# Kernel tuning notes

Measured on AMD Instinct MI355X. Metric: run time of the kernel, lower is better.

## Reference

```python
import jax, jax.numpy as jnp
import numpy as np

# ---- dims ----
B0, CIN, Hh, Ww = 8, 256, 96, 96
SPLIT = 8
DM = CIN // SPLIT            # 32  per-split d_model
EXPAND = 2
DIN = EXPAND * DM            # 64  d_inner
DSTATE = 64
DCONV = 3
HEADDIM = 8
NH = DIN // HEADDIM          # 8 heads
DOUT = 256
CHUNK = 32
D_IN_PROJ = 2 * DIN + 2 * DSTATE + NH  # 264
CONV_CH = DIN + 2 * DSTATE   # 192


def setup_inputs() -> dict:
    key = jax.random.key(0)
    ks = jax.random.split(key, 10)
    x = jax.random.normal(ks[0], (B0, CIN, Hh, Ww), jnp.float32)
    inp = {
        'x': x,
        'ln_w': jnp.ones((CIN,), jnp.float32),
        'ln_b': jnp.zeros((CIN,), jnp.float32),
        'skip_scale': jnp.ones((1,), jnp.float32),
        'proj_w': jax.random.normal(ks[1], (CIN, DOUT), jnp.float32) / np.sqrt(CIN),
        'proj_b': jnp.zeros((DOUT,), jnp.float32),
        'W_in': jax.random.normal(ks[2], (DM, D_IN_PROJ), jnp.float32) / np.sqrt(DM),
        'conv_w': jax.random.normal(ks[3], (CONV_CH, 1, DCONV), jnp.float32) * 0.3,
        'conv_b': jnp.zeros((CONV_CH,), jnp.float32),
        'dt_bias': jax.random.normal(ks[4], (NH,), jnp.float32) * 0.5,
        'A_log': jnp.log(jnp.arange(1.0, NH + 1.0, dtype=jnp.float32)),
        'D': jax.random.normal(ks[5], (NH,), jnp.float32) * 0.5,
        'rms_w': jnp.ones((DIN,), jnp.float32),
        'W_out': jax.random.normal(ks[6], (DIN, DM), jnp.float32) / np.sqrt(DIN),
    }
    return inp


def _layernorm(x, w, b, eps=1e-5):
    mu = jnp.mean(x, -1, keepdims=True)
    xc = x - mu
    var = jnp.mean(xc * xc, -1, keepdims=True)
    return xc * jax.lax.rsqrt(var + eps) * w + b


def _ssd(x, A, Bm, Cm, chunk):
    # x: (b,l,h,p)  A: (b,l,h)  Bm/Cm: (b,l,n); chunked SSD (Mamba2 minimal)
    b, l, h, p = x.shape
    n = Bm.shape[-1]
    nc = l // chunk
    xc = x.reshape(b, nc, chunk, h, p)
    Ac = A.reshape(b, nc, chunk, h).transpose(0, 3, 1, 2)  # (b,h,c,l)
    Bc = Bm.reshape(b, nc, chunk, n)
    Cc = Cm.reshape(b, nc, chunk, n)
    ac = jnp.cumsum(Ac, -1)                                 # (b,h,c,l)
    seg = ac[..., :, None] - ac[..., None, :]
    mask = jnp.tril(jnp.ones((chunk, chunk), bool))
    L = jnp.where(mask, jnp.exp(jnp.where(mask, seg, 0.0)), 0.0)  # (b,h,c,l,s)
    Yd = jnp.einsum('bcln,bcsn,bhcls,bcshp->bclhp', Cc, Bc, L, xc)
    decay_states = jnp.exp(ac[..., -1:] - ac)               # (b,h,c,l)
    states = jnp.einsum('bcln,bhcl,bclhp->bchpn', Bc, decay_states, xc)
    chunk_decay = jnp.exp(ac[..., -1])                      # (b,h,c)
    def step(carry, inp):
        s, d = inp
        return carry * d[..., None, None] + s, carry
    states_t = jnp.moveaxis(states, 1, 0)                   # (c,b,h,p,n)
    dec_t = jnp.moveaxis(chunk_decay, 2, 0)                 # (c,b,h)
    _, prev = jax.lax.scan(step, jnp.zeros_like(states_t[0]), (states_t, dec_t))
    prev = jnp.moveaxis(prev, 0, 1)                         # (b,c,h,p,n)
    Yo = jnp.einsum('bcln,bchpn,bhcl->bclhp', Cc, prev, jnp.exp(ac))
    return (Yd + Yo).reshape(b, l, h, p)


def _mamba2(u, W_in, conv_w, conv_b, dt_bias, A_log, D, rms_w, W_out):
    b, l, _ = u.shape
    zxbcdt = u @ W_in
    z = zxbcdt[..., :DIN]
    xBC = zxbcdt[..., DIN:DIN + CONV_CH]
    dt = jax.nn.softplus(zxbcdt[..., -NH:] + dt_bias)       # (b,l,h)
    conv = jax.lax.conv_general_dilated(
        xBC.transpose(0, 2, 1), conv_w, (1,), [(DCONV - 1, 0)],
        dimension_numbers=('NCH', 'OIH', 'NCH'), feature_group_count=CONV_CH)
    xBC = jax.nn.silu(conv + conv_b[None, :, None]).transpose(0, 2, 1)
    xs = xBC[..., :DIN].reshape(b, l, NH, HEADDIM)
    Bm = xBC[..., DIN:DIN + DSTATE]
    Cm = xBC[..., DIN + DSTATE:]
    A = -jnp.exp(A_log)
    y = _ssd(xs * dt[..., None], dt * A, Bm, Cm, CHUNK)
    y = y + xs * D[None, None, :, None]
    y = y.reshape(b, l, DIN) * jax.nn.silu(z)               # gated
    y = y * jax.lax.rsqrt(jnp.mean(y * y, -1, keepdims=True) + 1e-5) * rms_w
    return y @ W_out


def reference(x, ln_w, ln_b, skip_scale, proj_w, proj_b, W_in, conv_w, conv_b,
              dt_bias, A_log, D, rms_w, W_out):
    Bn, C, h, w = x.shape
    L = h * w
    xf = x.reshape(Bn, C, L).transpose(0, 2, 1)             # (B,L,C)
    xn = _layernorm(xf, ln_w, ln_b)
    d = C // SPLIT
    xs = jnp.moveaxis(xn.reshape(Bn, L, SPLIT, d), 2, 0)    # (S,B,L,d)
    xs = xs.reshape(SPLIT * Bn, L, d)
    ym = _mamba2(xs, W_in, conv_w, conv_b, dt_bias, A_log, D, rms_w, W_out)
    ym = ym + skip_scale * xs
    ym = jnp.moveaxis(ym.reshape(SPLIT, Bn, L, d), 0, 2).reshape(Bn, L, C)
    ym = _layernorm(ym, ln_w, ln_b)
    out = ym @ proj_w + proj_b                              # (B,L,DOUT)
    return out.transpose(0, 2, 1).reshape(Bn, DOUT, h, w)
```

## Files before the change

### kernel.cpp

```cpp
#include <hip/hip_runtime.h>
#include <hip/hip_fp16.h>
#include <math.h>

typedef unsigned short u16;
typedef unsigned int u32;
typedef _Float16 half2_t __attribute__((ext_vector_type(2)));
typedef _Float16 f16x8 __attribute__((ext_vector_type(8)));
typedef float f32x4 __attribute__((ext_vector_type(4)));

#define B0N 8
#define LSEQ 9216
#define NSEQ 64
#define NCHUNK 288
#define DM 32
#define DPROJ 264
#define CONVCH 192
#define XC4 208
#define URH 40
#define CHH 204
#define ZBS 66
#define C2H 132
#define TTS 40
#define GS 36
#define YH5 264

#ifndef __has_builtin
#define __has_builtin(x) 0
#endif

__device__ __forceinline__ float silu_(float v) { return v / (1.f + __expf(-v)); }

__global__ __launch_bounds__(256) void k1_ln_split(const float* __restrict__ x,
                                                   const float* __restrict__ lnw,
                                                   const float* __restrict__ lnb,
                                                   __half* __restrict__ u) {
  __shared__ float tile[256 * 33];
  __shared__ float mu[32], rs[32], wv[256], bv[256];
  __shared__ float ps[32 * 9], ps2[32 * 9];
  const int b = blockIdx.y, l0 = blockIdx.x * 32, t = threadIdx.x;
  wv[t] = lnw[t];
  bv[t] = lnb[t];
#pragma unroll
  for (int i = 0; i < 8; ++i) {
    int idx = i * 256 + t;
    int cc = idx >> 3, part = idx & 7;
    float4 v = *(const float4*)&x[((size_t)b * 256 + cc) * LSEQ + l0 + part * 4];
    tile[cc * 33 + part * 4 + 0] = v.x;
    tile[cc * 33 + part * 4 + 1] = v.y;
    tile[cc * 33 + part * 4 + 2] = v.z;
    tile[cc * 33 + part * 4 + 3] = v.w;
  }
  __syncthreads();
  {
    const int ll = t & 31, seg = t >> 5;
    float s = 0.f, s2 = 0.f;
#pragma unroll 8
    for (int i = 0; i < 32; ++i) {
      float v = tile[(seg * 32 + i) * 33 + ll];
      s += v; s2 += v * v;
    }
    ps[ll * 9 + seg] = s;
    ps2[ll * 9 + seg] = s2;
  }
  __syncthreads();
  if (t < 32) {
    float s = 0.f, s2 = 0.f;
#pragma unroll
    for (int seg = 0; seg < 8; ++seg) { s += ps[t * 9 + seg]; s2 += ps2[t * 9 + seg]; }
    float m = s * (1.f / 256.f);
    mu[t] = m;
    rs[t] = rsqrtf(s2 * (1.f / 256.f) - m * m + 1e-5f);
  }
  __syncthreads();
#pragma unroll 4
  for (int i = 0; i < 32; ++i) {
    int sp = i >> 2, sub = i & 3;
    int ll = sub * 8 + (t >> 5), dm = t & 31;
    int c = sp * 32 + dm;
    float v = (tile[c * 33 + ll] - mu[ll]) * rs[ll] * wv[c] + bv[c];
    u[(((size_t)(sp * B0N + b)) * LSEQ + l0 + ll) * DM + dm] = __float2half(v);
  }
}

__global__ __launch_bounds__(256, 4) void k2_states(
    const __half* __restrict__ u, const float* __restrict__ Win,
    const float* __restrict__ convw, const float* __restrict__ convb,
    const float* __restrict__ dtbias, const float* __restrict__ Alog,
    __half* __restrict__ S, float* __restrict__ cdec) {
  __shared__ __align__(16) char smem[32512];
  _Float16* ur_h = (_Float16*)smem;
  _Float16* CH2h = (_Float16*)(smem + 3840);
  _Float16* Ah   = (_Float16*)(smem + 3840);
  __half*   Sout = (__half*)(smem + 8960);
  _Float16* xst  = (_Float16*)(smem + 18176);
  _Float16* Bt   = (_Float16*)(smem + 23296);
  float* dtraw = (float*)(smem + 28416);
  float* dtv   = (float*)(smem + 29440);
  float* acs   = (float*)(smem + 30464);
  float* wv2   = (float*)(smem + 31488);
  const int c = blockIdx.x, sq = blockIdx.y, t = threadIdx.x;
  const int l0 = c * 32;
  const int lane = t & 63, wvi = t >> 6, g = lane >> 4, c16 = lane & 15;
  const size_t ubase = (size_t)sq * (LSEQ * DM);
  const f32x4 zero4 = {0.f, 0.f, 0.f, 0.f};

  for (int idx = t; idx < 48 * 32; idx += 256) {
    int r = idx >> 5, dm = idx & 31;
    int l = l0 - 2 + r;
    _Float16 v = (_Float16)0.f;
    if (r < 34 && l >= 0) v = ((const _Float16*)u)[ubase + (size_t)l * DM + dm];
    ur_h[r * URH + dm] = v;
  }
  f16x8 bfr[2];
#pragma unroll
  for (int i = 0; i < 2; ++i) {
    int col = 64 + (wvi + i * 4) * 16 + c16;
#pragma unroll
    for (int j = 0; j < 8; ++j) bfr[i][j] = (_Float16)Win[(g * 8 + j) * DPROJ + col];
  }
  __syncthreads();

  {
    f16x8 am[3];
#pragma unroll
    for (int mt = 0; mt < 3; ++mt)
      am[mt] = *(const f16x8*)&ur_h[(mt * 16 + c16) * URH + g * 8];
#pragma unroll
    for (int i = 0; i < 2; ++i) {
      int colc = (wvi + i * 4) * 16 + c16;
#pragma unroll
      for (int mt = 0; mt < 3; ++mt) {
        f32x4 acc = __builtin_amdgcn_mfma_f32_16x16x32_f16(am[mt], bfr[i], zero4, 0, 0, 0);
#pragma unroll
        for (int r = 0; r < 4; ++r) {
          int R = mt * 16 + 4 * g + r;
          if (R < 34) CH2h[R * C2H + colc] = (_Float16)acc[r];
        }
      }
    }
  }
  __syncthreads();

  {
    const int ch0 = t & 63, lbq = t >> 6;
#pragma unroll
    for (int cr = 0; cr < 2; ++cr) {
      int ch = ch0 + cr * 64;
      float w0 = convw[ch * 3 + 0], w1 = convw[ch * 3 + 1], w2 = convw[ch * 3 + 2];
      float cb = convb[ch];
      float a = (float)CH2h[(lbq * 8 + 0) * C2H + ch];
      float b = (float)CH2h[(lbq * 8 + 1) * C2H + ch];
      f16x8 out;
#pragma unroll
      for (int j = 0; j < 8; ++j) {
        float cn = (float)CH2h[(lbq * 8 + j + 2) * C2H + ch];
        out[j] = (_Float16)silu_(a * w0 + b * w1 + cn * w2 + cb);
        a = b; b = cn;
      }
      if (cr == 0) *(f16x8*)&xst[ch0 * TTS + lbq * 8] = out;
      else         *(f16x8*)&Bt[ch0 * TTS + lbq * 8] = out;
    }
    int l = t >> 3, h = t & 7;
    float raw = 0.f;
#pragma unroll
    for (int dm = 0; dm < 32; ++dm)
      raw += (float)ur_h[(l + 2) * URH + dm] * Win[dm * DPROJ + 256 + h];
    dtraw[l * 8 + h] = raw;
  }
  __syncthreads();

  {
    const int l = t & 31, h = t >> 5;
    float raw = dtraw[l * 8 + h] + dtbias[h];
    float dt = (raw > 20.f) ? raw : log1pf(__expf(raw));
    float x = dt;
#pragma unroll
    for (int d = 1; d < 32; d <<= 1) {
      float y = __shfl_up(x, d, 32);
      if (l >= d) x += y;
    }
    const float A = -__expf(Alog[h]);
    dtv[t] = dt;
    acs[t] = A * x;
    if (l == 31) cdec[(sq * NCHUNK + c) * 8 + h] = __expf(A * x);
  }
  __syncthreads();

  {
    int h = t >> 5;
    wv2[t] = __expf(acs[h * 32 + 31] - acs[t]) * dtv[t];
  }
  __syncthreads();
  {
    const int hp = t >> 2, lb2 = (t & 3) * 8;
    const float* w = &wv2[(hp >> 3) * 32 + lb2];
    const _Float16* xr = &xst[hp * TTS + lb2];
    f16x8 ov;
#pragma unroll
    for (int i = 0; i < 8; ++i) ov[i] = (_Float16)((float)xr[i] * w[i]);
    *(f16x8*)&Ah[hp * TTS + lb2] = ov;
  }
  __syncthreads();

  {
    const int mt = wvi;
    f16x8 aS = *(const f16x8*)&Ah[(mt * 16 + c16) * TTS + g * 8];
#pragma unroll
    for (int nt = 0; nt < 4; ++nt) {
      f16x8 bS = *(const f16x8*)&Bt[(nt * 16 + c16) * TTS + g * 8];
      f32x4 acc = __builtin_amdgcn_mfma_f32_16x16x32_f16(aS, bS, zero4, 0, 0, 0);
#pragma unroll
      for (int r = 0; r < 4; ++r)
        Sout[(mt * 16 + 4 * g + r) * 72 + nt * 16 + c16] = __float2half(acc[r]);
    }
  }
  __syncthreads();
  const size_t sbase = (size_t)(sq * NCHUNK + c) * 4096;
#pragma unroll
  for (int i = 0; i < 2; ++i) {
    int idx = i * 256 + t;
    int hp = idx >> 3, part = idx & 7;
    *(uint4*)(S + sbase + hp * 64 + part * 8) = *(const uint4*)&Sout[hp * 72 + part * 8];
  }
}

__global__ __launch_bounds__(256) void k3_scan(__half* __restrict__ S,
                                               const float* __restrict__ cdec) {
  __shared__ float cd[NCHUNK];
  const int sq = blockIdx.x >> 3, h = blockIdx.x & 7, t = threadIdx.x;
  for (int i = t; i < NCHUNK; i += 256) cd[i] = cdec[(sq * NCHUNK + i) * 8 + h];
  __syncthreads();
  __half* p = S + (size_t)sq * NCHUNK * 4096 + h * 512 + t * 2;
  u32 f0 = *(const u32*)(p);
  u32 f1 = *(const u32*)(p + 4096);
  u32 f2 = *(const u32*)(p + 2 * 4096);
  u32 f3 = *(const u32*)(p + 3 * 4096);
  u32 f4 = *(const u32*)(p + 4 * 4096);
  u32 f5 = *(const u32*)(p + 5 * 4096);
  u32 f6 = *(const u32*)(p + 6 * 4096);
  u32 f7 = *(const u32*)(p + 7 * 4096);
  float car0 = 0.f, car1 = 0.f;
  for (int c = 0; c < NCHUNK; c += 8) {
#define K3_STEP(F, K)                                                    \
    {                                                                    \
      half2_t s2h = *(half2_t*)&F;                                       \
      float s0 = (float)s2h.x, s1 = (float)s2h.y;                        \
      int nc = c + K + 8; if (nc > NCHUNK - 1) nc = NCHUNK - 1;          \
      F = *(const u32*)(p + (size_t)nc * 4096);                          \
      half2_t o; o.x = (_Float16)car0; o.y = (_Float16)car1;             \
      *(u32*)(p + (size_t)(c + K) * 4096) = *(u32*)&o;                   \
      float d = cd[c + K];                                               \
      car0 = car0 * d + s0; car1 = car1 * d + s1;                        \
    }
    K3_STEP(f0, 0)
    K3_STEP(f1, 1)
    K3_STEP(f2, 2)
    K3_STEP(f3, 3)
    K3_STEP(f4, 4)
    K3_STEP(f5, 5)
    K3_STEP(f6, 6)
    K3_STEP(f7, 7)
#undef K3_STEP
  }
}

__global__ __launch_bounds__(256, 4) void k4_out(
    const __half* __restrict__ u, const float* __restrict__ Win,
    const float* __restrict__ convw, const float* __restrict__ convb,
    const float* __restrict__ dtbias, const float* __restrict__ Alog,
    const float* __restrict__ Dp, const float* __restrict__ rmsw,
    const float* __restrict__ Wout, const float* __restrict__ skip,
    const __half* __restrict__ S, __half* __restrict__ ym) {
  __shared__ __align__(16) _Float16 ur_h[48 * URH];
  __shared__ __align__(16) _Float16 CHh[34 * CHH];
  __shared__ __align__(16) __half xch[32 * XC4];
  __shared__ __align__(16) float dtraw[256];
  __shared__ __align__(16) float dtv[256], acs[256];
  __shared__ __align__(16) _Float16 zbuf[32 * ZBS];
  const int c = blockIdx.x, sq = blockIdx.y, t = threadIdx.x;
  const int l0 = c * 32;
  const int lane = t & 63, wvi = t >> 6, g = lane >> 4, c16 = lane & 15;
  const size_t ubase = (size_t)sq * (LSEQ * DM);
  const f32x4 zero4 = {0.f, 0.f, 0.f, 0.f};

  const size_t sbase = (size_t)(sq * NCHUNK + c) * 4096;
  uint4 sv0, sv1;
  {
    const uint4* sp = (const uint4*)(S + sbase);
    sv0 = sp[t * 2];
    sv1 = sp[t * 2 + 1];
  }
  for (int idx = t; idx < 48 * 32; idx += 256) {
    int r = idx >> 5, dm = idx & 31;
    int l = l0 - 2 + r;
    _Float16 v = (_Float16)0.f;
    if (r < 34 && l >= 0) v = ((const _Float16*)u)[ubase + (size_t)l * DM + dm];
    ur_h[r * URH + dm] = v;
  }
  f16x8 bfr[3];
#pragma unroll
  for (int i = 0; i < 3; ++i) {
    int col = 64 + (wvi + i * 4) * 16 + c16;
#pragma unroll
    for (int j = 0; j < 8; ++j) bfr[i][j] = (_Float16)Win[(g * 8 + j) * DPROJ + col];
  }
  f16x8 bz;
  {
    int col = wvi * 16 + c16;
#pragma unroll
    for (int j = 0; j < 8; ++j) bz[j] = (_Float16)Win[(g * 8 + j) * DPROJ + col];
  }
  __syncthreads();

  {
    f16x8 am[3];
#pragma unroll
    for (int mt = 0; mt < 3; ++mt)
      am[mt] = *(const f16x8*)&ur_h[(mt * 16 + c16) * URH + g * 8];
#pragma unroll
    for (int i = 0; i < 3; ++i) {
      int colc = (wvi + i * 4) * 16 + c16;
#pragma unroll
      for (int mt = 0; mt < 3; ++mt) {
        f32x4 acc = __builtin_amdgcn_mfma_f32_16x16x32_f16(am[mt], bfr[i], zero4, 0, 0, 0);
#pragma unroll
        for (int r = 0; r < 4; ++r) {
          int R = mt * 16 + 4 * g + r;
          if (R < 34) CHh[R * CHH + colc] = (_Float16)acc[r];
        }
      }
    }
#pragma unroll
    for (int mz = 0; mz < 2; ++mz) {
      f16x8 az = *(const f16x8*)&ur_h[(2 + mz * 16 + c16) * URH + g * 8];
      f32x4 acc = __builtin_amdgcn_mfma_f32_16x16x32_f16(az, bz, zero4, 0, 0, 0);
#pragma unroll
      for (int r = 0; r < 4; ++r) {
        int lY = mz * 16 + 4 * g + r;
        zbuf[lY * ZBS + wvi * 16 + c16] = (_Float16)acc[r];
      }
    }
  }
  __syncthreads();

  {
    const int ch0 = t & 63, lbq = t >> 6;
#pragma unroll
    for (int cr = 0; cr < 3; ++cr) {
      int ch = ch0 + cr * 64;
      float w0 = convw[ch * 3 + 0], w1 = convw[ch * 3 + 1], w2 = convw[ch * 3 + 2];
      float cb = convb[ch];
      float a = (float)CHh[(lbq * 8 + 0) * CHH + ch];
      float b = (float)CHh[(lbq * 8 + 1) * CHH + ch];
#pragma unroll
      for (int j = 0; j < 8; ++j) {
        float cn = (float)CHh[(lbq * 8 + j + 2) * CHH + ch];
        float v = a * w0 + b * w1 + cn * w2 + cb;
        xch[(lbq * 8 + j) * XC4 + ch] = __float2half(silu_(v));
        a = b; b = cn;
      }
    }
    int l = t >> 3, h = t & 7;
    float raw = 0.f;
#pragma unroll
    for (int dm = 0; dm < 32; ++dm)
      raw += (float)ur_h[(l + 2) * URH + dm] * Win[dm * DPROJ + 256 + h];
    dtraw[l * 8 + h] = raw;
  }
  __syncthreads();

  {
    char* pvb = (char*)CHh;
    int hp = t >> 2, part = t & 3;
    *(uint4*)(pvb + hp * 144 + part * 32) = sv0;
    *(uint4*)(pvb + hp * 144 + part * 32 + 16) = sv1;
  }
  {
    const int l = t & 31, h = t >> 5;
    float raw = dtraw[l * 8 + h] + dtbias[h];
    float dt = (raw > 20.f) ? raw : log1pf(__expf(raw));
    float x = dt;
#pragma unroll
    for (int d = 1; d < 32; d <<= 1) {
      float y = __shfl_up(x, d, 32);
      if (l >= d) x += y;
    }
    dtv[t] = dt;
    acs[t] = -__expf(Alog[h]) * x;
  }
  __syncthreads();

  float* Gm = (float*)((char*)CHh + 9216);
  {
    float ev = __expf(acs[t]);
    dtraw[t] = ev;
    const int mt = wvi >> 1, nt = wvi & 1;
    f32x4 acc = zero4;
#pragma unroll
    for (int kk = 0; kk < 2; ++kk) {
      f16x8 aC = *(const f16x8*)&xch[(mt * 16 + c16) * XC4 + 128 + kk * 32 + g * 8];
      f16x8 bB = *(const f16x8*)&xch[(nt * 16 + c16) * XC4 + 64 + kk * 32 + g * 8];
      acc = __builtin_amdgcn_mfma_f32_16x16x32_f16(aC, bB, acc, 0, 0, 0);
    }
#pragma unroll
    for (int r = 0; r < 4; ++r)
      Gm[(mt * 16 + 4 * g + r) * GS + nt * 16 + c16] = acc[r];
  }
  __syncthreads();

  {
    const int s2b = g * 8;
    float gv[2][8];
#pragma unroll
    for (int mt = 0; mt < 2; ++mt) {
      const float* gr = &Gm[(mt * 16 + c16) * GS + s2b];
      float4 g0 = *(const float4*)gr;
      float4 g1 = *(const float4*)(gr + 4);
      gv[mt][0] = g0.x; gv[mt][1] = g0.y; gv[mt][2] = g0.z; gv[mt][3] = g0.w;
      gv[mt][4] = g1.x; gv[mt][5] = g1.y; gv[mt][6] = g1.z; gv[mt][7] = g1.w;
    }
#pragma unroll
    for (int hh = 0; hh < 2; ++hh) {
      const int h = 2 * wvi + hh;
      const float* ap = &acs[h * 32 + s2b];
      const float* dp = &dtv[h * 32 + s2b];
      float4 a0 = *(const float4*)ap, a1 = *(const float4*)(ap + 4);
      float4 d0 = *(const float4*)dp, d1 = *(const float4*)(dp + 4);
      const float av[8] = {a0.x, a0.y, a0.z, a0.w, a1.x, a1.y, a1.z, a1.w};
      const float dv[8] = {d0.x, d0.y, d0.z, d0.w, d1.x, d1.y, d1.z, d1.w};
      f16x8 bfr2;
#pragma unroll
      for (int j = 0; j < 8; ++j)
        bfr2[j] = *(const _Float16*)&xch[(s2b + j) * XC4 + h * 8 + (c16 & 7)];
#pragma unroll
      for (int mt = 0; mt < 2; ++mt) {
        const int row = mt * 16 + c16;
        const float arow = acs[h * 32 + row];
        f16x8 afr;
#pragma unroll
        for (int j = 0; j < 8; ++j) {
          float m = gv[mt][j] * __expf(arow - av[j]) * dv[j];
          afr[j] = (_Float16)((s2b + j <= row) ? m : 0.f);
        }
        f32x4 dacc = __builtin_amdgcn_mfma_f32_16x16x32_f16(afr, bfr2, zero4, 0, 0, 0);
        if (c16 < 8) {
#pragma unroll
          for (int r = 0; r < 4; ++r)
            xch[(mt * 16 + 4 * g + r) * XC4 + 64 + h * 8 + c16] = __float2half(dacc[r]);
        }
      }
    }
  }
  __syncthreads();

  {
    const __half* pvh = (const __half*)CHh;
#pragma unroll
    for (int mt = 0; mt < 2; ++mt) {
      f32x4 acc = zero4;
#pragma unroll
      for (int kk = 0; kk < 2; ++kk) {
        f16x8 aC = *(const f16x8*)&xch[(mt * 16 + c16) * XC4 + 128 + kk * 32 + g * 8];
        f16x8 bP = *(const f16x8*)&pvh[(wvi * 16 + c16) * 72 + kk * 32 + g * 8];
        acc = __builtin_amdgcn_mfma_f32_16x16x32_f16(aC, bP, acc, 0, 0, 0);
      }
      int hp = wvi * 16 + c16;
#pragma unroll
      for (int r = 0; r < 4; ++r) {
        int l = mt * 16 + 4 * g + r;
        float e = dtraw[(hp >> 3) * 32 + l];
        __half* yb = &xch[l * XC4 + 64 + hp];
        *yb = __float2half(__half2float(*yb) + acc[r] * e);
      }
    }
  }
  __syncthreads();

  {
    const int hp = t & 63;
    const float dcoef = Dp[hp >> 3];
#pragma unroll
    for (int k = 0; k < 8; ++k) {
      int l = (k * 256 + t) >> 6;
      float y = __half2float(xch[l * XC4 + 64 + hp]) + (float)xch[l * XC4 + hp] * dcoef;
      float z = (float)zbuf[l * ZBS + hp];
      y *= z / (1.f + __expf(-z));
      xch[l * XC4 + 64 + hp] = __float2half(y);
    }
  }
  __syncthreads();

  float* rp = Gm;
  float* scl = (float*)ur_h;
  {
    const int l = t & 31, seg = t >> 5;
    float p = 0.f;
#pragma unroll
    for (int k = 0; k < 8; ++k) {
      float v = __half2float(xch[l * XC4 + 64 + seg * 8 + k]);
      p += v * v;
    }
    rp[l * 9 + seg] = p;
  }
  __syncthreads();
  if (t < 32) {
    float s2s = 0.f;
#pragma unroll
    for (int seg = 0; seg < 8; ++seg) s2s += rp[t * 9 + seg];
    scl[t] = rsqrtf(s2s * (1.f / 64.f) + 1e-5f);
  }
  __syncthreads();

  for (int idx = t; idx < 2048; idx += 256) {
    int l = idx >> 6, hp = idx & 63;
    xch[l * XC4 + 64 + hp] =
        __float2half(__half2float(xch[l * XC4 + 64 + hp]) * scl[l] * rmsw[hp]);
  }
  __syncthreads();

  {
    const float skipv = skip[0];
    const int mt = wvi >> 1, nt = wvi & 1;
    f32x4 acc = zero4;
#pragma unroll
    for (int kk = 0; kk < 2; ++kk) {
      f16x8 aY = *(const f16x8*)&xch[(mt * 16 + c16) * XC4 + 64 + kk * 32 + g * 8];
      f16x8 bW;
#pragma unroll
      for (int j = 0; j < 8; ++j)
        bW[j] = (_Float16)Wout[(kk * 32 + g * 8 + j) * 32 + nt * 16 + c16];
      acc = __builtin_amdgcn_mfma_f32_16x16x32_f16(aY, bW, acc, 0, 0, 0);
    }
#pragma unroll
    for (int r = 0; r < 4; ++r) {
      int l = mt * 16 + 4 * g + r;
      int dm = nt * 16 + c16;
      size_t gi = ubase + (size_t)(l0 + l) * DM + dm;
      ym[gi] = __float2half(acc[r] + skipv * __half2float(u[gi]));
    }
  }
}

__global__ __launch_bounds__(256, 4) void k5_ln_proj(const __half* __restrict__ ym,
                                                     const float* __restrict__ lnw,
                                                     const float* __restrict__ lnb,
                                                     const float* __restrict__ pw,
                                                     const float* __restrict__ pb,
                                                     float* __restrict__ outp) {
  __shared__ __align__(16) char buf[33792];
  __shared__ float mu[32], rs[32], wv[256], bv[256];
  __shared__ float ps[32 * 9], ps2[32 * 9];
  _Float16* yh = (_Float16*)buf;
  float* res = (float*)buf;
  const int b = blockIdx.y, l0 = blockIdx.x * 32, t = threadIdx.x;
  const int lane = t & 63, wvi = t >> 6, g = lane >> 4, c16 = lane & 15;
  const f32x4 zero4 = {0.f, 0.f, 0.f, 0.f};
  wv[t] = lnw[t];
  bv[t] = lnb[t];
#pragma unroll
  for (int i = 0; i < 4; ++i) {
    int idx = i * 256 + t;
    int sp = idx >> 7, rem = idx & 127, ll = rem >> 2, part = rem & 3;
    uint4 v = *(const uint4*)&ym[(((size_t)(sp * B0N + b)) * LSEQ + l0 + ll) * DM + part * 8];
    *(uint4*)&yh[ll * YH5 + sp * 32 + part * 8] = v;
  }
  __syncthreads();
  {
    const int ll = t & 31, seg = t >> 5;
    float s = 0.f, s2 = 0.f;
#pragma unroll 8
    for (int i = 0; i < 32; ++i) {
      float v = (float)yh[ll * YH5 + seg * 32 + i];
      s += v; s2 += v * v;
    }
    ps[ll * 9 + seg] = s;
    ps2[ll * 9 + seg] = s2;
  }
  __syncthreads();
  if (t < 32) {
    float s = 0.f, s2 = 0.f;
#pragma unroll
    for (int seg = 0; seg < 8; ++seg) { s += ps[t * 9 + seg]; s2 += ps2[t * 9 + seg]; }
    float m = s * (1.f / 256.f);
    mu[t] = m;
    rs[t] = rsqrtf(s2 * (1.f / 256.f) - m * m + 1e-5f);
  }
  __syncthreads();
#pragma unroll
  for (int i = 0; i < 32; ++i) {
    int idx = i * 256 + t;
    int ll = idx >> 8, ch = idx & 255;
    float v = ((float)yh[ll * YH5 + ch] - mu[ll]) * rs[ll] * wv[ch] + bv[ch];
    yh[ll * YH5 + ch] = (_Float16)v;
  }
  __syncthreads();
  f16x8 am[16];
#pragma unroll
  for (int mt = 0; mt < 2; ++mt)
#pragma unroll
    for (int kk = 0; kk < 8; ++kk)
      am[mt * 8 + kk] = *(const f16x8*)&yh[(mt * 16 + c16) * YH5 + kk * 32 + g * 8];
  __syncthreads();
#pragma unroll
  for (int ni = 0; ni < 4; ++ni) {
    const int col = (wvi + ni * 4) * 16 + c16;
    f32x4 acc0 = zero4, acc1 = zero4;
#pragma unroll
    for (int kk = 0; kk < 8; ++kk) {
      f16x8 bW;
#pragma unroll
      for (int j = 0; j < 8; ++j)
        bW[j] = (_Float16)pw[(size_t)(kk * 32 + g * 8 + j) * 256 + col];
      acc0 = __builtin_amdgcn_mfma_f32_16x16x32_f16(am[kk], bW, acc0, 0, 0, 0);
      acc1 = __builtin_amdgcn_mfma_f32_16x16x32_f16(am[8 + kk], bW, acc1, 0, 0, 0);
    }
    const float bias = pb[col];
#pragma unroll
    for (int r = 0; r < 4; ++r) {
      res[col * 33 + 4 * g + r] = acc0[r] + bias;
      res[col * 33 + 16 + 4 * g + r] = acc1[r] + bias;
    }
  }
  __syncthreads();
  for (int idx = t; idx < 8192; idx += 256) {
    int o = idx >> 5, l = idx & 31;
    outp[((size_t)(b * 256 + o)) * LSEQ + l0 + l] = res[o * 33 + l];
  }
}

extern "C" void kernel_launch(void* const* d_in, const int* in_sizes, int n_in,
                              void* d_out, int out_size, void* d_ws, size_t ws_size,
                              hipStream_t stream) {
  (void)in_sizes; (void)n_in; (void)out_size;
  const float* x     = (const float*)d_in[0];
  const float* lnw   = (const float*)d_in[1];
  const float* lnb   = (const float*)d_in[2];
  const float* skip  = (const float*)d_in[3];
  const float* pw    = (const float*)d_in[4];
  const float* pb    = (const float*)d_in[5];
  const float* Win   = (const float*)d_in[6];
  const float* convw = (const float*)d_in[7];
  const float* convb = (const float*)d_in[8];
  const float* dtb   = (const float*)d_in[9];
  const float* Alog  = (const float*)d_in[10];
  const float* Dp    = (const float*)d_in[11];
  const float* rmsw  = (const float*)d_in[12];
  const float* Wout  = (const float*)d_in[13];
  float* outp = (float*)d_out;

  const size_t NEED = 227082240ull;
  if (ws_size < NEED) return;
  char* ws = (char*)d_ws;
  __half* u    = (__half*)ws;
  __half* S    = (__half*)(ws + 37748736);
  float*  cdec = (float*)(ws + 188743680);
  __half* ym   = (__half*)(ws + 189333504);

  k1_ln_split<<<dim3(288, 8), 256, 0, stream>>>(x, lnw, lnb, u);
  k2_states<<<dim3(288, 64), 256, 0, stream>>>(u, Win, convw, convb, dtb, Alog, S, cdec);
  k3_scan<<<dim3(512), 256, 0, stream>>>(S, cdec);
  k4_out<<<dim3(288, 64), 256, 0, stream>>>(u, Win, convw, convb, dtb, Alog, Dp, rmsw,
                                            Wout, skip, S, ym);
  k5_ln_proj<<<dim3(288, 8), 256, 0, stream>>>(ym, lnw, lnb, pw, pb, outp);
}
```

Baseline: 631.0 us.

## Transpose conv staging buffer, fuse SSD diagonal, state and gating epilogues via shuffles

Stores the in-projection MFMA output transposed, one row per channel, so the depthwise conv reads each channel's window with vector loads instead of strided scalar loads. In k4, the diagonal-block SSD result stays in registers and reaches the state-contribution pass through lane shuffles, so the D-skip and SiLU gate are applied in one epilogue. This drops two shared-memory round trips and two barriers. SiLU also switches to a hardware reciprocal, which changes rounding slightly.

```diff
diff --git a/kernel.cpp b/kernel.cpp
--- a/kernel.cpp
+++ b/kernel.cpp
@@ -5,6 +5,7 @@
 typedef unsigned short u16;
 typedef unsigned int u32;
 typedef _Float16 half2_t __attribute__((ext_vector_type(2)));
+typedef _Float16 f16x4 __attribute__((ext_vector_type(4)));
 typedef _Float16 f16x8 __attribute__((ext_vector_type(8)));
 typedef float f32x4 __attribute__((ext_vector_type(4)));
 
@@ -17,9 +18,8 @@
 #define CONVCH 192
 #define XC4 208
 #define URH 40
-#define CHH 204
+#define CTS 40
 #define ZBS 66
-#define C2H 132
 #define TTS 40
 #define GS 36
 #define YH5 264
@@ -28,7 +28,9 @@
 #define __has_builtin(x) 0
 #endif
 
-__device__ __forceinline__ float silu_(float v) { return v / (1.f + __expf(-v)); }
+__device__ __forceinline__ float silu_(float v) {
+  return v * __builtin_amdgcn_rcpf(1.f + __expf(-v));
+}
 
 __global__ __launch_bounds__(256) void k1_ln_split(const float* __restrict__ x,
                                                    const float* __restrict__ lnw,
@@ -89,7 +91,7 @@
     __half* __restrict__ S, float* __restrict__ cdec) {
   __shared__ __align__(16) char smem[32512];
   _Float16* ur_h = (_Float16*)smem;
-  _Float16* CH2h = (_Float16*)(smem + 3840);
+  _Float16* CH2T = (_Float16*)(smem + 3840);
   _Float16* Ah   = (_Float16*)(smem + 3840);
   __half*   Sout = (__half*)(smem + 8960);
   _Float16* xst  = (_Float16*)(smem + 18176);
@@ -131,10 +133,15 @@
 #pragma unroll
       for (int mt = 0; mt < 3; ++mt) {
         f32x4 acc = __builtin_amdgcn_mfma_f32_16x16x32_f16(am[mt], bfr[i], zero4, 0, 0, 0);
-#pragma unroll
-        for (int r = 0; r < 4; ++r) {
-          int R = mt * 16 + 4 * g + r;
-          if (R < 34) CH2h[R * C2H + colc] = (_Float16)acc[r];
+        if (mt < 2) {
+          f16x4 o;
+          o[0] = (_Float16)acc[0]; o[1] = (_Float16)acc[1];
+          o[2] = (_Float16)acc[2]; o[3] = (_Float16)acc[3];
+          *(f16x4*)&CH2T[colc * CTS + mt * 16 + 4 * g] = o;
+        } else if (g == 0) {
+          half2_t o;
+          o.x = (_Float16)acc[0]; o.y = (_Float16)acc[1];
+          *(half2_t*)&CH2T[colc * CTS + 32] = o;
         }
       }
     }
@@ -148,15 +155,16 @@
       int ch = ch0 + cr * 64;
       float w0 = convw[ch * 3 + 0], w1 = convw[ch * 3 + 1], w2 = convw[ch * 3 + 2];
       float cb = convb[ch];
-      float a = (float)CH2h[(lbq * 8 + 0) * C2H + ch];
-      float b = (float)CH2h[(lbq * 8 + 1) * C2H + ch];
+      f16x8 v8 = *(const f16x8*)&CH2T[ch * CTS + lbq * 8];
+      half2_t v2 = *(const half2_t*)&CH2T[ch * CTS + lbq * 8 + 8];
+      float v[10];
+#pragma unroll
+      for (int j = 0; j < 8; ++j) v[j] = (float)v8[j];
+      v[8] = (float)v2.x; v[9] = (float)v2.y;
       f16x8 out;
 #pragma unroll
-      for (int j = 0; j < 8; ++j) {
-        float cn = (float)CH2h[(lbq * 8 + j + 2) * C2H + ch];
-        out[j] = (_Float16)silu_(a * w0 + b * w1 + cn * w2 + cb);
-        a = b; b = cn;
-      }
+      for (int j = 0; j < 8; ++j)
+        out[j] = (_Float16)silu_(v[j] * w0 + v[j + 1] * w1 + v[j + 2] * w2 + cb);
       if (cr == 0) *(f16x8*)&xst[ch0 * TTS + lbq * 8] = out;
       else         *(f16x8*)&Bt[ch0 * TTS + lbq * 8] = out;
     }
@@ -272,7 +280,7 @@
     const float* __restrict__ Wout, const float* __restrict__ skip,
     const __half* __restrict__ S, __half* __restrict__ ym) {
   __shared__ __align__(16) _Float16 ur_h[48 * URH];
-  __shared__ __align__(16) _Float16 CHh[34 * CHH];
+  __shared__ __align__(16) _Float16 CHhT[192 * CTS];
   __shared__ __align__(16) __half xch[32 * XC4];
   __shared__ __align__(16) float dtraw[256];
   __shared__ __align__(16) float dtv[256], acs[256];
@@ -323,10 +331,15 @@
 #pragma unroll
       for (int mt = 0; mt < 3; ++mt) {
         f32x4 acc = __builtin_amdgcn_mfma_f32_16x16x32_f16(am[mt], bfr[i], zero4, 0, 0, 0);
-#pragma unroll
-        for (int r = 0; r < 4; ++r) {
-          int R = mt * 16 + 4 * g + r;
-          if (R < 34) CHh[R * CHH + colc] = (_Float16)acc[r];
+        if (mt < 2) {
+          f16x4 o;
+          o[0] = (_Float16)acc[0]; o[1] = (_Float16)acc[1];
+          o[2] = (_Float16)acc[2]; o[3] = (_Float16)acc[3];
+          *(f16x4*)&CHhT[colc * CTS + mt * 16 + 4 * g] = o;
+        } else if (g == 0) {
+          half2_t o;
+          o.x = (_Float16)acc[0]; o.y = (_Float16)acc[1];
+          *(half2_t*)&CHhT[colc * CTS + 32] = o;
         }
       }
     }
@@ -350,14 +363,16 @@
       int ch = ch0 + cr * 64;
       float w0 = convw[ch * 3 + 0], w1 = convw[ch * 3 + 1], w2 = convw[ch * 3 + 2];
       float cb = convb[ch];
-      float a = (float)CHh[(lbq * 8 + 0) * CHH + ch];
-      float b = (float)CHh[(lbq * 8 + 1) * CHH + ch];
+      f16x8 v8 = *(const f16x8*)&CHhT[ch * CTS + lbq * 8];
+      half2_t v2 = *(const half2_t*)&CHhT[ch * CTS + lbq * 8 + 8];
+      float v[10];
+#pragma unroll
+      for (int j = 0; j < 8; ++j) v[j] = (float)v8[j];
+      v[8] = (float)v2.x; v[9] = (float)v2.y;
 #pragma unroll
       for (int j = 0; j < 8; ++j) {
-        float cn = (float)CHh[(lbq * 8 + j + 2) * CHH + ch];
-        float v = a * w0 + b * w1 + cn * w2 + cb;
-        xch[(lbq * 8 + j) * XC4 + ch] = __float2half(silu_(v));
-        a = b; b = cn;
+        float s = v[j] * w0 + v[j + 1] * w1 + v[j + 2] * w2 + cb;
+        xch[(lbq * 8 + j) * XC4 + ch] = __float2half(silu_(s));
       }
     }
     int l = t >> 3, h = t & 7;
@@ -370,7 +385,7 @@
   __syncthreads();
 
   {
-    char* pvb = (char*)CHh;
+    char* pvb = (char*)CHhT;
     int hp = t >> 2, part = t & 3;
     *(uint4*)(pvb + hp * 144 + part * 32) = sv0;
     *(uint4*)(pvb + hp * 144 + part * 32 + 16) = sv1;
@@ -390,7 +405,7 @@
   }
   __syncthreads();
 
-  float* Gm = (float*)((char*)CHh + 9216);
+  float* Gm = (float*)((char*)CHhT + 9216);
   {
     float ev = __expf(acs[t]);
     dtraw[t] = ev;
@@ -408,6 +423,7 @@
   }
   __syncthreads();
 
+  float dacc[2][2][4];
   {
     const int s2b = g * 8;
     float gv[2][8];
@@ -442,19 +458,18 @@
           float m = gv[mt][j] * __expf(arow - av[j]) * dv[j];
           afr[j] = (_Float16)((s2b + j <= row) ? m : 0.f);
         }
-        f32x4 dacc = __builtin_amdgcn_mfma_f32_16x16x32_f16(afr, bfr2, zero4, 0, 0, 0);
-        if (c16 < 8) {
-#pragma unroll
-          for (int r = 0; r < 4; ++r)
-            xch[(mt * 16 + 4 * g + r) * XC4 + 64 + h * 8 + c16] = __float2half(dacc[r]);
-        }
+        f32x4 d = __builtin_amdgcn_mfma_f32_16x16x32_f16(afr, bfr2, zero4, 0, 0, 0);
+#pragma unroll
+        for (int r = 0; r < 4; ++r) dacc[hh][mt][r] = d[r];
       }
     }
   }
-  __syncthreads();
-
-  {
-    const __half* pvh = (const __half*)CHh;
+
+  {
+    const __half* pvh = (const __half*)CHhT;
+    const int hp = wvi * 16 + c16;
+    const float dcoef = Dp[hp >> 3];
+    const int srcLane = g * 16 + (c16 & 7);
 #pragma unroll
     for (int mt = 0; mt < 2; ++mt) {
       f32x4 acc = zero4;
@@ -464,28 +479,19 @@
         f16x8 bP = *(const f16x8*)&pvh[(wvi * 16 + c16) * 72 + kk * 32 + g * 8];
         acc = __builtin_amdgcn_mfma_f32_16x16x32_f16(aC, bP, acc, 0, 0, 0);
       }
-      int hp = wvi * 16 + c16;
 #pragma unroll
       for (int r = 0; r < 4; ++r) {
         int l = mt * 16 + 4 * g + r;
+        float yd0 = __shfl(dacc[0][mt][r], srcLane, 64);
+        float yd1 = __shfl(dacc[1][mt][r], srcLane, 64);
+        float yd = (c16 < 8) ? yd0 : yd1;
         float e = dtraw[(hp >> 3) * 32 + l];
-        __half* yb = &xch[l * XC4 + 64 + hp];
-        *yb = __float2half(__half2float(*yb) + acc[r] * e);
+        float xs = __half2float(xch[l * XC4 + hp]);
+        float y = yd + acc[r] * e + xs * dcoef;
+        float z = (float)zbuf[l * ZBS + hp];
+        y *= z * __builtin_amdgcn_rcpf(1.f + __expf(-z));
+        xch[l * XC4 + 64 + hp] = __float2half(y);
       }
-    }
-  }
-  __syncthreads();
-
-  {
-    const int hp = t & 63;
-    const float dcoef = Dp[hp >> 3];
-#pragma unroll
-    for (int k = 0; k < 8; ++k) {
-      int l = (k * 256 + t) >> 6;
-      float y = __half2float(xch[l * XC4 + 64 + hp]) + (float)xch[l * XC4 + hp] * dcoef;
-      float z = (float)zbuf[l * ZBS + hp];
-      y *= z / (1.f + __expf(-z));
-      xch[l * XC4 + 64 + hp] = __float2half(y);
     }
   }
   __syncthreads();
```

After: 587.7 us. 1.07x faster.
